# Optimization experiments

Measured on AMD Instinct MI355X. Metric: run time of the kernel, lower is better.

## Reference

```python
import jax, jax.numpy as jnp
import numpy as np

N, E, H, R = 50000, 800000, 256, 8
LN_EPS = 1e-5


def setup_inputs() -> dict:
    key = jax.random.key(0)
    ks = jax.random.split(key, 6)
    node_states = jax.random.normal(ks[0], (N, H), dtype=jnp.float32)
    edge_index = jax.random.randint(ks[1], (2, E), 0, N, dtype=jnp.int64)
    edge_type_ids = jax.random.randint(ks[2], (E,), 0, R, dtype=jnp.int64)
    scale = 1.0 / np.sqrt(H)
    W_rel = jax.random.normal(ks[3], (R, H, H), dtype=jnp.float32) * scale
    W_root = jax.random.normal(ks[4], (H, H), dtype=jnp.float32) * scale
    bias = jnp.zeros((H,), dtype=jnp.float32)
    ln_gamma = jnp.ones((H,), dtype=jnp.float32)
    ln_beta = jnp.zeros((H,), dtype=jnp.float32)
    return {
        "node_states": node_states,
        "edge_index": edge_index,
        "edge_type_ids": edge_type_ids,
        "W_rel": W_rel,
        "W_root": W_root,
        "bias": bias,
        "ln_gamma": ln_gamma,
        "ln_beta": ln_beta,
    }


def _rgcn_layer(node_states, edge_index, edge_type_ids, W_rel, W_root, bias, ln_gamma, ln_beta):
    n, h = node_states.shape
    r = W_rel.shape[0]
    src, dst = edge_index[0], edge_index[1]
    # Per-(dst, relation) MEAN of source features (PyG RGCNConv default aggr='mean').
    seg = dst * r + edge_type_ids  # composite segment id in [0, N*R)
    msgs = node_states[src]  # [E, H] gather
    sums = jax.ops.segment_sum(msgs, seg, num_segments=n * r).reshape(n, r, h)
    counts = jax.ops.segment_sum(jnp.ones((src.shape[0],), node_states.dtype), seg,
                                 num_segments=n * r).reshape(n, r, 1)
    mean = sums / jnp.maximum(counts, 1.0)  # zero-edge buckets stay 0
    # Relation-specific linear transforms applied to aggregated means, then root + bias.
    agg = jnp.einsum('nrh,rho->no', mean, W_rel)
    conv = agg + node_states @ W_root + bias
    # Exact (erf-based) GELU to match torch.nn.functional.gelu default.
    updated = jax.nn.gelu(conv, approximate=False)
    # Dropout is identity in eval mode.
    x = updated + node_states  # residual
    mu = jnp.mean(x, axis=-1, keepdims=True)
    var = jnp.mean(jnp.square(x - mu), axis=-1, keepdims=True)
    return ln_gamma * (x - mu) * jax.lax.rsqrt(var + LN_EPS) + ln_beta


def reference(node_states, edge_index, edge_type_ids, W_rel, W_root, bias, ln_gamma, ln_beta):
    return _rgcn_layer(node_states, edge_index, edge_type_ids, W_rel, W_root, bias, ln_gamma, ln_beta)
```

## Files before the change

kernel.cpp:

```cpp
#include <hip/hip_runtime.h>
#include <cstdint>
#include <cstddef>

#define N_NODES 50000
#define N_EDGES 800000
#define HDIM    256
#define NREL    8
#define NSEG    (N_NODES * NREL)
#define KDIM    (NREL * HDIM + HDIM)
#define KA      (NREL * HDIM)
#define LN_EPSF 1e-5f

#define SCAN_CHUNK 1024
#define SCAN_NB    ((NSEG + SCAN_CHUNK - 1) / SCAN_CHUNK)

using short8  = __attribute__((ext_vector_type(8))) short;
using ushort8 = __attribute__((ext_vector_type(8))) unsigned short;
using float4v = __attribute__((ext_vector_type(4))) float;

static __device__ __forceinline__ unsigned short f2bf(float f) {
    union { float f; uint32_t i; } v; v.f = f;
    uint32_t r = v.i + 0x7FFFu + ((v.i >> 16) & 1u);
    return (unsigned short)(r >> 16);
}
static __device__ __forceinline__ float bf2f(unsigned short u) {
    union { uint32_t i; float f; } v; v.i = ((uint32_t)u) << 16; return v.f;
}

__global__ __launch_bounds__(256) void k_cast(const float* __restrict__ ns,
                                              unsigned short* __restrict__ ns16) {
    int idx = blockIdx.x * blockDim.x + threadIdx.x;
    if (idx >= N_NODES * HDIM / 8) return;
    const float4v* nsv = (const float4v*)ns;
    float4v v0 = nsv[idx * 2], v1 = nsv[idx * 2 + 1];
    ushort8 o;
    o[0] = f2bf(v0[0]); o[1] = f2bf(v0[1]); o[2] = f2bf(v0[2]); o[3] = f2bf(v0[3]);
    o[4] = f2bf(v1[0]); o[5] = f2bf(v1[1]); o[6] = f2bf(v1[2]); o[7] = f2bf(v1[3]);
    *(ushort8*)&ns16[(size_t)idx * 8] = o;
}

__global__ void k_count(const int* __restrict__ ei, const int* __restrict__ et,
                        int* __restrict__ cnt) {
    int e = blockIdx.x * blockDim.x + threadIdx.x;
    if (e >= N_EDGES) return;
    int dst = ei[N_EDGES + e];
    int rel = et[e];
    atomicAdd(&cnt[dst * NREL + rel], 1);
}

__global__ __launch_bounds__(256) void k_scan1(const int* __restrict__ cnt,
                                               int* __restrict__ bsum) {
    int b = blockIdx.x, t = threadIdx.x;
    int idx = b * SCAN_CHUNK + t * 4;
    int4 v = {0, 0, 0, 0};
    if (idx + 3 < NSEG) v = *(const int4*)&cnt[idx];
    else {
        #pragma unroll
        for (int j = 0; j < 4; ++j) if (idx + j < NSEG) ((int*)&v)[j] = cnt[idx + j];
    }
    int s = v.x + v.y + v.z + v.w;
    #pragma unroll
    for (int o = 32; o > 0; o >>= 1) s += __shfl_xor(s, o, 64);
    __shared__ int ls[4];
    if ((t & 63) == 0) ls[t >> 6] = s;
    __syncthreads();
    if (t == 0) bsum[b] = ls[0] + ls[1] + ls[2] + ls[3];
}

__global__ __launch_bounds__(512) void k_scan2(const int* __restrict__ bsum,
                                               int* __restrict__ boff) {
    __shared__ int s[512];
    int t = threadIdx.x;
    int v = (t < SCAN_NB) ? bsum[t] : 0;
    s[t] = v;
    __syncthreads();
    for (int d = 1; d < 512; d <<= 1) {
        int x = (t >= d) ? s[t - d] : 0;
        __syncthreads();
        s[t] += x;
        __syncthreads();
    }
    if (t < SCAN_NB) boff[t] = s[t] - v;
}

__global__ __launch_bounds__(256) void k_scan3(const int* __restrict__ cnt,
                                               const int* __restrict__ boff,
                                               int* __restrict__ off) {
    int b = blockIdx.x, t = threadIdx.x;
    int idx = b * SCAN_CHUNK + t * 4;
    int4 v = {0, 0, 0, 0};
    if (idx + 3 < NSEG) v = *(const int4*)&cnt[idx];
    else {
        #pragma unroll
        for (int j = 0; j < 4; ++j) if (idx + j < NSEG) ((int*)&v)[j] = cnt[idx + j];
    }
    int s = v.x + v.y + v.z + v.w;
    __shared__ int ls[256];
    ls[t] = s;
    __syncthreads();
    for (int d = 1; d < 256; d <<= 1) {
        int x = (t >= d) ? ls[t - d] : 0;
        __syncthreads();
        ls[t] += x;
        __syncthreads();
    }
    int run = boff[b] + ls[t] - s;
    int4 w;
    w.x = run; run += v.x;
    w.y = run; run += v.y;
    w.z = run; run += v.z;
    w.w = run;
    if (idx + 3 < NSEG) *(int4*)&off[idx] = w;
    else {
        #pragma unroll
        for (int j = 0; j < 4; ++j) if (idx + j < NSEG) off[idx + j] = ((int*)&w)[j];
    }
    if (b == 0 && t == 0) off[NSEG] = N_EDGES;
}

__global__ void k_scatter(const int* __restrict__ ei, const int* __restrict__ et,
                          const int* __restrict__ off, int* __restrict__ cursor,
                          int* __restrict__ srcs) {
    int e = blockIdx.x * blockDim.x + threadIdx.x;
    if (e >= N_EDGES) return;
    int src = ei[e];
    int dst = ei[N_EDGES + e];
    int rel = et[e];
    int seg = dst * NREL + rel;
    int pos = off[seg] + atomicAdd(&cursor[seg], 1);
    srcs[pos] = src;
}

__global__ __launch_bounds__(256) void k_aggregate(const unsigned short* __restrict__ ns16,
                                                   const int* __restrict__ off,
                                                   const int* __restrict__ srcs,
                                                   unsigned short* __restrict__ Afull) {
    int n = blockIdx.x, t = threadIdx.x;
    int g = t >> 5;
    int i = t & 31;
    int seg = n * NREL + g;
    int e0 = off[seg], e1 = off[seg + 1];
    int cnt = e1 - e0;
    int cs = cnt < 32 ? cnt : 32;
    int my_src = (i < cs) ? srcs[e0 + i] : 0;

    const ushort8* nsv = (const ushort8*)ns16;
    float acc[8] = {0.f, 0.f, 0.f, 0.f, 0.f, 0.f, 0.f, 0.f};

    for (int k = 0; k < cs; ++k) {
        int src = __shfl(my_src, k, 32);
        ushort8 v = nsv[(size_t)src * 32 + i];
        #pragma unroll
        for (int j = 0; j < 8; ++j) acc[j] += bf2f(v[j]);
    }
    for (int e = e0 + 32; e < e1; ++e) {
        int src = srcs[e];
        ushort8 v = nsv[(size_t)src * 32 + i];
        #pragma unroll
        for (int j = 0; j < 8; ++j) acc[j] += bf2f(v[j]);
    }

    float inv = (cnt > 0) ? 1.0f / (float)cnt : 0.0f;
    ushort8 wv;
    #pragma unroll
    for (int j = 0; j < 8; ++j) wv[j] = f2bf(acc[j] * inv);
    *(ushort8*)&Afull[(size_t)n * KA + g * HDIM + i * 8] = wv;
}

__global__ __launch_bounds__(256) void k_buildB(const float* __restrict__ Wrel,
                                                const float* __restrict__ Wroot,
                                                unsigned short* __restrict__ Bt) {
    __shared__ unsigned short tile[64][66];
    int k0 = blockIdx.x * 64;
    int j0 = blockIdx.y * 64;
    int t = threadIdx.x;

    #pragma unroll
    for (int p = 0; p < 16; ++p) {
        int idx = p * 256 + t;
        int kk = idx >> 6, jj = idx & 63;
        int k = k0 + kk;
        float v;
        if (k < NREL * HDIM) {
            int r = k >> 8, h = k & 255;
            v = Wrel[((size_t)r * HDIM + h) * HDIM + (j0 + jj)];
        } else {
            int h = k - NREL * HDIM;
            v = Wroot[(size_t)h * HDIM + (j0 + jj)];
        }
        tile[kk][jj] = f2bf(v);
    }
    __syncthreads();
    #pragma unroll
    for (int p = 0; p < 16; ++p) {
        int idx = p * 256 + t;
        int jj = idx >> 6, kk = idx & 63;
        Bt[(size_t)(j0 + jj) * KDIM + (k0 + kk)] = tile[kk][jj];
    }
}

#define BM 128
#define BN 256
#define BK 64
#define NITER (KDIM / BK)

__global__ __launch_bounds__(512, 4) void k_gemm(const unsigned short* __restrict__ A,
                                                 const unsigned short* __restrict__ ns16,
                                                 const unsigned short* __restrict__ Bt,
                                                 const float* __restrict__ ns,
                                                 const float* __restrict__ bias,
                                                 const float* __restrict__ gamma,
                                                 const float* __restrict__ beta,
                                                 float* __restrict__ out, int M) {
    __shared__ __align__(16) unsigned short As[BM * BK];
    __shared__ __align__(16) unsigned short Bs[BN * BK];
    __shared__ float s1buf[BM][4], s2buf[BM][4];

    int tid  = threadIdx.x;
    int lane = tid & 63;
    int wid  = tid >> 6;
    int wm   = wid >> 2, wn = wid & 3;
    int brow = blockIdx.x * BM;

    float4v acc[4][4] = {};

    const char* Ab = (const char*)A;
    const char* Nb = (const char*)ns16;
    const char* Bb = (const char*)Bt;
    const size_t rstrideA = (size_t)KA * 2;
    const size_t rstrideB = (size_t)KDIM * 2;

    for (int kt = 0; kt < KDIM; kt += BK) {
        #pragma unroll
        for (int i = 0; i < 2; ++i) {
            int linear = i * 8192 + tid * 16;
            int row  = linear >> 7;
            int slot = (linear >> 4) & 7;
            int kb   = (slot ^ (row & 7)) * 16;
            int ra = brow + row; if (ra > M - 1) ra = M - 1;
            const char* ga = (kt < KA)
                ? Ab + (size_t)ra * rstrideA + (size_t)(kt * 2 + kb)
                : Nb + (size_t)ra * (HDIM * 2) + (size_t)((kt - KA) * 2 + kb);
            __builtin_amdgcn_global_load_lds(
                (const __attribute__((address_space(1))) void*)ga,
                (__attribute__((address_space(3))) void*)((char*)As + linear),
                16, 0, 0);
        }
        #pragma unroll
        for (int i = 0; i < 4; ++i) {
            int linear = i * 8192 + tid * 16;
            int row  = linear >> 7;
            int slot = (linear >> 4) & 7;
            int kb   = (slot ^ (row & 7)) * 16;
            const char* gb = Bb + (size_t)row * rstrideB + (size_t)(kt * 2 + kb);
            __builtin_amdgcn_global_load_lds(
                (const __attribute__((address_space(1))) void*)gb,
                (__attribute__((address_space(3))) void*)((char*)Bs + linear),
                16, 0, 0);
        }
        __syncthreads();

        #pragma unroll
        for (int h = 0; h < 2; ++h) {
            short8 a[4], b[4];
            int s0 = h * 4 + (lane >> 4);
            #pragma unroll
            for (int m = 0; m < 4; ++m) {
                int r = wm * 64 + m * 16 + (lane & 15);
                a[m] = *(const short8*)((const char*)As + r * 128 + ((s0 ^ (r & 7)) * 16));
            }
            #pragma unroll
            for (int n = 0; n < 4; ++n) {
                int r = wn * 64 + n * 16 + (lane & 15);
                b[n] = *(const short8*)((const char*)Bs + r * 128 + ((s0 ^ (r & 7)) * 16));
            }
            #pragma unroll
            for (int m = 0; m < 4; ++m)
                #pragma unroll
                for (int n = 0; n < 4; ++n)
                    acc[m][n] = __builtin_amdgcn_mfma_f32_16x16x32_bf16(a[m], b[n], acc[m][n], 0, 0, 0);
        }
        __syncthreads();
    }

    int cols[4];
    float bias_v[4];
    #pragma unroll
    for (int n = 0; n < 4; ++n) {
        cols[n] = wn * 64 + n * 16 + (lane & 15);
        bias_v[n] = bias[cols[n]];
    }

    #pragma unroll
    for (int m = 0; m < 4; ++m) {
        #pragma unroll
        for (int q = 0; q < 4; ++q) {
            int lr = wm * 64 + m * 16 + (lane >> 4) * 4 + q;
            int r  = brow + lr;
            float s1 = 0.f, s2 = 0.f;
            #pragma unroll
            for (int n = 0; n < 4; ++n) {
                float conv = acc[m][n][q] + bias_v[n];
                float g = 0.5f * conv * (1.0f + erff(conv * 0.70710678118654752f));
                float resid = (r < M) ? ns[(size_t)r * HDIM + cols[n]] : 0.f;
                float x = g + resid;
                acc[m][n][q] = x;
                s1 += x; s2 += x * x;
            }
            #pragma unroll
            for (int o = 8; o > 0; o >>= 1) {
                s1 += __shfl_xor(s1, o, 64);
                s2 += __shfl_xor(s2, o, 64);
            }
            if ((lane & 15) == 0) { s1buf[lr][wn] = s1; s2buf[lr][wn] = s2; }
        }
    }
    __syncthreads();

    float gam[4], bet[4];
    #pragma unroll
    for (int n = 0; n < 4; ++n) { gam[n] = gamma[cols[n]]; bet[n] = beta[cols[n]]; }

    #pragma unroll
    for (int m = 0; m < 4; ++m) {
        #pragma unroll
        for (int q = 0; q < 4; ++q) {
            int lr = wm * 64 + m * 16 + (lane >> 4) * 4 + q;
            int r  = brow + lr;
            float t1 = s1buf[lr][0] + s1buf[lr][1] + s1buf[lr][2] + s1buf[lr][3];
            float t2 = s2buf[lr][0] + s2buf[lr][1] + s2buf[lr][2] + s2buf[lr][3];
            float mu  = t1 * (1.0f / HDIM);
            float var = t2 * (1.0f / HDIM) - mu * mu;
            float rstd = rsqrtf(var + LN_EPSF);
            if (r < M) {
                #pragma unroll
                for (int n = 0; n < 4; ++n) {
                    float x = acc[m][n][q];
                    out[(size_t)r * HDIM + cols[n]] = gam[n] * (x - mu) * rstd + bet[n];
                }
            }
        }
    }
}

extern "C" void kernel_launch(void* const* d_in, const int* in_sizes, int n_in,
                              void* d_out, int out_size, void* d_ws, size_t ws_size,
                              hipStream_t stream) {
    const float* ns    = (const float*)d_in[0];
    const int*   ei    = (const int*)d_in[1];
    const int*   et    = (const int*)d_in[2];
    const float* Wrel  = (const float*)d_in[3];
    const float* Wroot = (const float*)d_in[4];
    const float* bias  = (const float*)d_in[5];
    const float* gamma = (const float*)d_in[6];
    const float* beta  = (const float*)d_in[7];
    float* out = (float*)d_out;

    char* w = (char*)d_ws;
    auto take = [&](size_t bytes) -> char* {
        char* p = w; w += (bytes + 255) & ~(size_t)255; return p;
    };
    int* cnt              = (int*)take((size_t)NSEG * 4);
    int* segoff           = (int*)take((size_t)(NSEG + 1) * 4);
    int* cursor           = (int*)take((size_t)NSEG * 4);
    int* srcs             = (int*)take((size_t)N_EDGES * 4);
    int* bsum             = (int*)take((size_t)SCAN_NB * 4);
    int* boff             = (int*)take((size_t)SCAN_NB * 4);
    unsigned short* Afull = (unsigned short*)take((size_t)N_NODES * KA * 2);
    unsigned short* Bt    = (unsigned short*)take((size_t)HDIM * KDIM * 2);
    unsigned short* ns16  = (unsigned short*)take((size_t)N_NODES * HDIM * 2);

    hipMemsetAsync(cnt, 0, (size_t)NSEG * 4, stream);
    hipMemsetAsync(cursor, 0, (size_t)NSEG * 4, stream);

    k_cast<<<(N_NODES * HDIM / 8 + 255) / 256, 256, 0, stream>>>(ns, ns16);
    k_count<<<(N_EDGES + 255) / 256, 256, 0, stream>>>(ei, et, cnt);
    k_scan1<<<SCAN_NB, 256, 0, stream>>>(cnt, bsum);
    k_scan2<<<1, 512, 0, stream>>>(bsum, boff);
    k_scan3<<<SCAN_NB, 256, 0, stream>>>(cnt, boff, segoff);
    k_scatter<<<(N_EDGES + 255) / 256, 256, 0, stream>>>(ei, et, segoff, cursor, srcs);
    k_aggregate<<<N_NODES, 256, 0, stream>>>(ns16, segoff, srcs, Afull);
    dim3 gb(KDIM / 64, HDIM / 64);
    k_buildB<<<gb, 256, 0, stream>>>(Wrel, Wroot, Bt);

    dim3 gg((N_NODES + BM - 1) / BM, 1);
    k_gemm<<<gg, 512, 0, stream>>>(Afull, ns16, Bt, ns, bias, gamma, beta, out, N_NODES);
}
```

Baseline: 312.3 us.

## Column-slice the aggregation so concurrent blocks share an L2-resident feature slice

The aggregation kernel is restructured so that each block handles a 32-column slice of the features for 256 nodes, with 4 lanes per (node, relation) segment, in place of one block per node covering all 256 columns. Blocks that run at the same time gather the same narrow column slice, which shrinks the working set of the random source-row gathers and should improve cache hit rates. The Afull buffer row stride becomes KDIM instead of KA, and the GEMM uses that one stride for both A and B. In exchange, each segment is split across only 4 lanes, so segments with many edges iterate serially and per-lane work is uneven.

```diff
diff --git a/kernel.cpp b/kernel.cpp
--- a/kernel.cpp
+++ b/kernel.cpp
@@ -13,6 +13,9 @@
 
 #define SCAN_CHUNK 1024
 #define SCAN_NB    ((NSEG + SCAN_CHUNK - 1) / SCAN_CHUNK)
+
+#define AG_SLICES 8
+#define AG_NPB    256
 
 using short8  = __attribute__((ext_vector_type(8))) short;
 using ushort8 = __attribute__((ext_vector_type(8))) unsigned short;
@@ -135,36 +138,44 @@
                                                    const int* __restrict__ off,
                                                    const int* __restrict__ srcs,
                                                    unsigned short* __restrict__ Afull) {
-    int n = blockIdx.x, t = threadIdx.x;
-    int g = t >> 5;
-    int i = t & 31;
-    int seg = n * NREL + g;
-    int e0 = off[seg], e1 = off[seg + 1];
-    int cnt = e1 - e0;
-    int cs = cnt < 32 ? cnt : 32;
-    int my_src = (i < cs) ? srcs[e0 + i] : 0;
-
-    const ushort8* nsv = (const ushort8*)ns16;
-    float acc[8] = {0.f, 0.f, 0.f, 0.f, 0.f, 0.f, 0.f, 0.f};
-
-    for (int k = 0; k < cs; ++k) {
-        int src = __shfl(my_src, k, 32);
-        ushort8 v = nsv[(size_t)src * 32 + i];
-        #pragma unroll
-        for (int j = 0; j < 8; ++j) acc[j] += bf2f(v[j]);
-    }
-    for (int e = e0 + 32; e < e1; ++e) {
-        int src = srcs[e];
-        ushort8 v = nsv[(size_t)src * 32 + i];
-        #pragma unroll
-        for (int j = 0; j < 8; ++j) acc[j] += bf2f(v[j]);
-    }
-
-    float inv = (cnt > 0) ? 1.0f / (float)cnt : 0.0f;
-    ushort8 wv;
-    #pragma unroll
-    for (int j = 0; j < 8; ++j) wv[j] = f2bf(acc[j] * inv);
-    *(ushort8*)&Afull[(size_t)n * KA + g * HDIM + i * 8] = wv;
+    int s   = blockIdx.x;
+    int n0  = blockIdx.y * AG_NPB;
+    int tid = threadIdx.x;
+    int eid = tid >> 2;
+    int l4  = tid & 3;
+    int rel = eid & 7;
+    int nodeoff = eid >> 3;
+    int colbase = s * 32 + l4 * 8;
+
+    for (int np = 0; np < AG_NPB; np += 8) {
+        int n = n0 + np + nodeoff;
+        if (n < N_NODES) {
+            int seg = n * NREL + rel;
+            int e0 = off[seg], e1 = off[seg + 1];
+            int cnt = e1 - e0;
+            int cs = cnt < 4 ? cnt : 4;
+            int my_src = (l4 < cs) ? srcs[e0 + l4] : 0;
+
+            float acc[8] = {0.f, 0.f, 0.f, 0.f, 0.f, 0.f, 0.f, 0.f};
+            for (int k = 0; k < cs; ++k) {
+                int src = __shfl(my_src, k, 4);
+                ushort8 v = *(const ushort8*)&ns16[(size_t)src * HDIM + colbase];
+                #pragma unroll
+                for (int j = 0; j < 8; ++j) acc[j] += bf2f(v[j]);
+            }
+            for (int e = e0 + 4; e < e1; ++e) {
+                int src = srcs[e];
+                ushort8 v = *(const ushort8*)&ns16[(size_t)src * HDIM + colbase];
+                #pragma unroll
+                for (int j = 0; j < 8; ++j) acc[j] += bf2f(v[j]);
+            }
+            float inv = (cnt > 0) ? 1.0f / (float)cnt : 0.0f;
+            ushort8 wv;
+            #pragma unroll
+            for (int j = 0; j < 8; ++j) wv[j] = f2bf(acc[j] * inv);
+            *(ushort8*)&Afull[(size_t)n * KDIM + rel * HDIM + colbase] = wv;
+        }
+    }
 }
 
 __global__ __launch_bounds__(256) void k_buildB(const float* __restrict__ Wrel,
@@ -227,8 +238,7 @@
     const char* Ab = (const char*)A;
     const char* Nb = (const char*)ns16;
     const char* Bb = (const char*)Bt;
-    const size_t rstrideA = (size_t)KA * 2;
-    const size_t rstrideB = (size_t)KDIM * 2;
+    const size_t rstride = (size_t)KDIM * 2;
 
     for (int kt = 0; kt < KDIM; kt += BK) {
         #pragma unroll
@@ -239,7 +249,7 @@
             int kb   = (slot ^ (row & 7)) * 16;
             int ra = brow + row; if (ra > M - 1) ra = M - 1;
             const char* ga = (kt < KA)
-                ? Ab + (size_t)ra * rstrideA + (size_t)(kt * 2 + kb)
+                ? Ab + (size_t)ra * rstride + (size_t)(kt * 2 + kb)
                 : Nb + (size_t)ra * (HDIM * 2) + (size_t)((kt - KA) * 2 + kb);
             __builtin_amdgcn_global_load_lds(
                 (const __attribute__((address_space(1))) void*)ga,
@@ -252,7 +262,7 @@
             int row  = linear >> 7;
             int slot = (linear >> 4) & 7;
             int kb   = (slot ^ (row & 7)) * 16;
-            const char* gb = Bb + (size_t)row * rstrideB + (size_t)(kt * 2 + kb);
+            const char* gb = Bb + (size_t)row * rstride + (size_t)(kt * 2 + kb);
             __builtin_amdgcn_global_load_lds(
                 (const __attribute__((address_space(1))) void*)gb,
                 (__attribute__((address_space(3))) void*)((char*)Bs + linear),
@@ -366,7 +376,7 @@
     int* srcs             = (int*)take((size_t)N_EDGES * 4);
     int* bsum             = (int*)take((size_t)SCAN_NB * 4);
     int* boff             = (int*)take((size_t)SCAN_NB * 4);
-    unsigned short* Afull = (unsigned short*)take((size_t)N_NODES * KA * 2);
+    unsigned short* Afull = (unsigned short*)take((size_t)N_NODES * KDIM * 2);
     unsigned short* Bt    = (unsigned short*)take((size_t)HDIM * KDIM * 2);
     unsigned short* ns16  = (unsigned short*)take((size_t)N_NODES * HDIM * 2);
 
@@ -379,7 +389,10 @@
     k_scan2<<<1, 512, 0, stream>>>(bsum, boff);
     k_scan3<<<SCAN_NB, 256, 0, stream>>>(cnt, boff, segoff);
     k_scatter<<<(N_EDGES + 255) / 256, 256, 0, stream>>>(ei, et, segoff, cursor, srcs);
-    k_aggregate<<<N_NODES, 256, 0, stream>>>(ns16, segoff, srcs, Afull);
+
+    dim3 ga(AG_SLICES, (N_NODES + AG_NPB - 1) / AG_NPB);
+    k_aggregate<<<ga, 256, 0, stream>>>(ns16, segoff, srcs, Afull);
+
     dim3 gb(KDIM / 64, HDIM / 64);
     k_buildB<<<gb, 256, 0, stream>>>(Wrel, Wroot, Bt);
 
```

Result: slower. 346.8 us (+11.1%).
